# Optimization experiments

Measured on AMD Instinct MI355X. Metric: run time of the kernel, lower is better.

Reference implementation:

```python
import jax, jax.numpy as jnp
import numpy as np

H, E, V, MAXLEN, PAD = 8, 256, 1024, 64, 0


def _ln(x, g, b, eps):
    m = jnp.mean(x, -1, keepdims=True)
    v = jnp.mean((x - m) ** 2, -1, keepdims=True)
    return (x - m) / jnp.sqrt(v + eps) * g + b


def _get_pos(max_len, emb_dim):
    # replicates SVTISDPA.get_pos (sinusoidal, freq built via cumprod)
    half = emb_dim // 2
    freq = jnp.full((half,), 10000.0 ** (-1.0 / half), dtype=jnp.float32).at[0].set(1.0)
    freq = jnp.cumprod(freq)
    phase = jnp.arange(max_len, dtype=jnp.float32)[:, None] * freq[None, :]
    pe = jnp.zeros((max_len, emb_dim), dtype=jnp.float32)
    pe = pe.at[:, 0::2].set(jnp.sin(phase)).at[:, 1::2].set(jnp.cos(phase))
    return pe


def setup_inputs() -> dict:
    key = jax.random.key(0)
    ks = jax.random.split(key, 4)
    char_code = jax.random.randint(ks[0], (512, 64), 0, V)  # [B, max_len]
    emb_w = (jax.random.normal(ks[1], (V, E), dtype=jnp.float32) * 0.05).at[PAD].set(0.0)
    qkv_w = jax.random.normal(ks[2], (3 * E * H, E), dtype=jnp.float32) * 0.05
    fc_w = jax.random.normal(ks[3], (E, E * H), dtype=jnp.float32) * 0.05
    return {
        'char_code': char_code,
        'emb_w': emb_w,
        'qkv_w': qkv_w,
        'fc_w': fc_w,
        'fc_b': jnp.zeros((E,), jnp.float32),
        'sdpa_ln_g': jnp.ones((E,), jnp.float32),
        'sdpa_ln_b': jnp.zeros((E,), jnp.float32),
        'ff_ln_g': jnp.ones((E,), jnp.float32),
        'ff_ln_b': jnp.zeros((E,), jnp.float32),
        'bn_g': jnp.ones((E,), jnp.float32),
        'bn_b': jnp.zeros((E,), jnp.float32),
        'max_len': 64,
    }


def reference(char_code, emb_w, qkv_w, fc_w, fc_b, sdpa_ln_g, sdpa_ln_b,
              ff_ln_g, ff_ln_b, bn_g, bn_b, max_len):
    temp = E ** 0.5
    pos = _get_pos(MAXLEN, E)

    def qkv(x):
        y = (x @ qkv_w.T).reshape(x.shape[0], H, 3 * E)
        return y[..., :E], y[..., E:2 * E], y[..., 2 * E:]

    cq, ck, cv = qkv(emb_w)   # each [V, H, E]
    pq, pk, pv = qkv(pos)     # each [L, H, E]

    char_qk = jnp.einsum('vhe,whe->hvw', cq, ck) / temp          # [H,V,V]
    char_qk = char_qk.at[:, :, PAD].set(-1e9)
    pos_qk = jnp.einsum('lhe,mhe->hlm', pq, pk) / temp           # [H,L,L]
    char_pos_qk = (jnp.einsum('vhe,lhe->hvl', cq, pk)
                   + jnp.einsum('lhe,vhe->hvl', pq, ck)) / temp  # [H,V,L]

    c = char_code[:, :max_len]  # [B,M]
    M = max_len
    # sim[b,h,i,j] = char_qk[h,c_bi,c_bj] + char_pos_qk[h,c_bi,j] + pos_qk[h,i,j]
    sim = (char_qk[:, c[:, :, None], c[:, None, :]]
           + char_pos_qk[:, c, :M]).transpose(1, 0, 2, 3) \
          + pos_qk[None, :, :M, :M]                              # [B,H,M,M]
    attn = jax.nn.softmax(sim, axis=-1)

    not_mask = (c != PAD).astype(sim.dtype)                      # [B,M]
    n_words = jnp.sum(not_mask, -1)                              # [B]
    pooled = jnp.einsum('bm,bhmj->bhj', not_mask, attn) / n_words[:, None, None]

    v = cv[c].transpose(0, 2, 1, 3) + pv.transpose(1, 0, 2)[None, :, :M]  # [B,H,M,E]
    out = jnp.einsum('bhm,bhme->bhe', pooled, v).reshape(c.shape[0], H * E)
    out = _ln(out @ fc_w.T + fc_b, sdpa_ln_g, sdpa_ln_b, 1e-5)
    # FeedForward.forward returns layer_norm(x) (residual branch is dead code)
    out = _ln(out, ff_ln_g, ff_ln_b, 1e-6) + out
    return _ln(out, bn_g, bn_b, 1e-5)
```

## Files before the change

### kernel.cpp

```cpp
#include <hip/hip_runtime.h>
#include <math.h>

typedef unsigned short u16;
typedef __attribute__((ext_vector_type(4))) float f32x4;
typedef __attribute__((ext_vector_type(8))) short s16x8;
typedef __attribute__((ext_vector_type(4))) unsigned short u16x4;
typedef __attribute__((ext_vector_type(8))) unsigned short u16x8;

__device__ __forceinline__ u16 f2b(float f) {
  union { float f; unsigned u; } v; v.f = f;
  return (u16)((v.u + 0x7fffu + ((v.u >> 16) & 1u)) >> 16);
}
__device__ __forceinline__ float b2f(u16 b) {
  union { unsigned u; float f; } v; v.u = ((unsigned)b) << 16;
  return v.f;
}

__global__ __launch_bounds__(256) void prep_kernel(
    const float* __restrict__ emb, const float* __restrict__ qkv,
    const float* __restrict__ fc,
    u16* __restrict__ emb_bf, u16* __restrict__ qkvw_bf, u16* __restrict__ fcx,
    u16* __restrict__ pe)
{
  const int bid = blockIdx.x;
  if (bid < 2304) {
    const int i = bid * 256 + threadIdx.x;
    if (i < 65536) {
      f32x4 v = *(const f32x4*)&emb[(size_t)i * 4];
      u16x4 o = { f2b(v[0]), f2b(v[1]), f2b(v[2]), f2b(v[3]) };
      *(u16x4*)&emb_bf[(size_t)i * 4] = o;
    } else if (i < 458752) {
      const int off = i - 65536;
      f32x4 v = *(const f32x4*)&qkv[(size_t)off * 4];
      u16x4 o = { f2b(v[0]), f2b(v[1]), f2b(v[2]), f2b(v[3]) };
      *(u16x4*)&qkvw_bf[(size_t)off * 4] = o;
    } else {
      const int off4 = (i - 458752) * 4;
      const int row = off4 >> 11, col = off4 & 2047;
      f32x4 v = *(const f32x4*)&fc[(size_t)off4];
      u16x4 o = { f2b(v[0]), f2b(v[1]), f2b(v[2]), f2b(v[3]) };
      *(u16x4*)&fcx[(size_t)row * 2560 + col] = o;
    }
  } else {
    const int t = threadIdx.x;
    const int m = (bid - 2304) * 2 + (t >> 7);
    const int k = t & 127;
    float sv = 0.f, cv = 0.f;
    if (m < 64) {
      double f = pow(10000.0, -(double)k / 128.0);
      float ph = (float)m * (float)f;
      sv = sinf(ph); cv = cosf(ph);
    }
    pe[m * 256 + 2 * k]     = f2b(sv);
    pe[m * 256 + 2 * k + 1] = f2b(cv);
  }
}

__global__ __launch_bounds__(256) void gemm128(
    const u16* __restrict__ emb, const u16* __restrict__ pe,
    const u16* __restrict__ B,
    u16* __restrict__ Ccq, u16* __restrict__ Cpq)
{
  __shared__ __align__(16) u16 As[128 * 64];
  __shared__ __align__(16) u16 Bs[128 * 64];
  const int ytile = blockIdx.y;
  const u16* A; u16* C; int m0;
  if (ytile < 8) { A = emb; C = Ccq; m0 = ytile * 128; }
  else           { A = pe;  C = Cpq; m0 = 0; }
  const int n0 = blockIdx.x * 128;
  const int tid = threadIdx.x;
  const int w = tid >> 6, l = tid & 63, hi = l >> 4, lo = l & 15;
  const int wr = (w >> 1) * 64, wc = (w & 1) * 64;
  const int srow = tid >> 3, scol = (tid & 7) * 8;
  f32x4 acc[4][4] = {};
  for (int k0 = 0; k0 < 256; k0 += 64) {
    __syncthreads();
    #pragma unroll
    for (int q = 0; q < 4; ++q) {
      const int row = q * 32 + srow;
      const int sidx = row * 64 + (scol ^ ((row & 7) << 3));
      *(u16x8*)&As[sidx] = *(const u16x8*)&A[(long)(m0 + row) * 256 + k0 + scol];
      *(u16x8*)&Bs[sidx] = *(const u16x8*)&B[(long)(n0 + row) * 256 + k0 + scol];
    }
    __syncthreads();
    #pragma unroll
    for (int kk = 0; kk < 2; ++kk) {
      s16x8 a[4], bf[4];
      #pragma unroll
      for (int m = 0; m < 4; ++m) {
        const int ar = wr + m * 16 + lo;
        a[m] = *(const s16x8*)&As[ar * 64 + ((hi * 8 + kk * 32) ^ ((ar & 7) << 3))];
      }
      #pragma unroll
      for (int n = 0; n < 4; ++n) {
        const int br = wc + n * 16 + lo;
        bf[n] = *(const s16x8*)&Bs[br * 64 + ((hi * 8 + kk * 32) ^ ((br & 7) << 3))];
      }
      #pragma unroll
      for (int m = 0; m < 4; ++m)
        #pragma unroll
        for (int n = 0; n < 4; ++n)
          acc[m][n] = __builtin_amdgcn_mfma_f32_16x16x32_bf16(a[m], bf[n], acc[m][n], 0, 0, 0);
    }
  }
  #pragma unroll
  for (int m = 0; m < 4; ++m)
    #pragma unroll
    for (int n = 0; n < 4; ++n)
      #pragma unroll
      for (int r = 0; r < 4; ++r)
        C[(long)(m0 + wr + m * 16 + hi * 4 + r) * 6144 + n0 + wc + n * 16 + lo] = f2b(acc[m][n][r]);
}

__global__ __launch_bounds__(256) void gemm_bf(
    const u16* __restrict__ A, int lda, long sA,
    const u16* __restrict__ B, int ldb, long sB,
    float* __restrict__ C, int ldc, long sC, int K)
{
  __shared__ __align__(16) u16 As[64 * 64];
  __shared__ __align__(16) u16 Bs[64 * 64];
  const int z = blockIdx.z;
  A += (long)z * sA;  B += (long)z * sB;
  const int m0 = blockIdx.y * 64, n0 = blockIdx.x * 64;
  const int tid = threadIdx.x;
  const int srow = tid >> 2, sq = tid & 3;
  const int w = tid >> 6, l = tid & 63, hi = l >> 4, lo = l & 15;
  f32x4 acc[4] = {};
  for (int k0 = 0; k0 < K; k0 += 64) {
    __syncthreads();
    #pragma unroll
    for (int p = 0; p < 2; ++p) {
      const int col = sq * 16 + p * 8;
      const int sidx = srow * 64 + (col ^ ((srow & 7) << 3));
      *(u16x8*)&As[sidx] = *(const u16x8*)&A[(long)(m0 + srow) * lda + k0 + col];
      *(u16x8*)&Bs[sidx] = *(const u16x8*)&B[(long)(n0 + srow) * ldb + k0 + col];
    }
    __syncthreads();
    #pragma unroll
    for (int kk = 0; kk < 2; ++kk) {
      const int arow = w * 16 + lo;
      s16x8 a = *(const s16x8*)&As[arow * 64 + ((hi * 8 + kk * 32) ^ ((arow & 7) << 3))];
      #pragma unroll
      for (int n = 0; n < 4; ++n) {
        const int brow = n * 16 + lo;
        s16x8 bfr = *(const s16x8*)&Bs[brow * 64 + ((hi * 8 + kk * 32) ^ ((brow & 7) << 3))];
        acc[n] = __builtin_amdgcn_mfma_f32_16x16x32_bf16(a, bfr, acc[n], 0, 0, 0);
      }
    }
  }
  const long zoff = (long)z * sC;
  #pragma unroll
  for (int n = 0; n < 4; ++n)
    #pragma unroll
    for (int r = 0; r < 4; ++r)
      C[zoff + (long)(m0 + w * 16 + hi * 4 + r) * ldc + n0 + n * 16 + lo] = acc[n][r];
}

__global__ __launch_bounds__(256) void tables_kernel(
    const u16* __restrict__ cqkv, const u16* __restrict__ pqkv,
    const u16* __restrict__ fcx,
    u16* __restrict__ cpqk, u16* __restrict__ pqk, u16* __restrict__ pvfc)
{
  __shared__ __align__(16) u16 As1[64 * 64], Bs1[64 * 64];
  __shared__ __align__(16) u16 As2[64 * 64], Bs2[64 * 64];
  const int blk = blockIdx.x;
  const u16 *A1, *A2 = nullptr, *B1, *B2 = nullptr;
  u16* C; int lda, ldb, ldc, m0; bool dual = false;
  if (blk < 128) {
    const int h = blk & 7, mt = blk >> 3;
    A1 = cqkv + h * 768 + 256; A2 = cqkv + h * 768;
    B1 = pqkv + h * 768;       B2 = pqkv + h * 768 + 256;
    lda = 6144; ldb = 6144; C = cpqk + (long)h * 65536; ldc = 64;
    m0 = mt * 64; dual = true;
  } else if (blk < 136) {
    const int h = blk - 128;
    A1 = pqkv + h * 768; B1 = pqkv + h * 768 + 256;
    lda = 6144; ldb = 6144; C = pqk + h * 4096; ldc = 64; m0 = 0;
  } else {
    const int idx = blk - 136, h = idx & 7, mt = idx >> 3;
    A1 = fcx + h * 256; B1 = pqkv + 512 + h * 768;
    lda = 2560; ldb = 6144; C = pvfc + h * 64; ldc = 2560; m0 = mt * 64;
  }
  const int tid = threadIdx.x;
  const int srow = tid >> 2, sq = tid & 3;
  const int w = tid >> 6, l = tid & 63, hi = l >> 4, lo = l & 15;
  f32x4 acc[4] = {};
  for (int k0 = 0; k0 < 256; k0 += 64) {
    __syncthreads();
    #pragma unroll
    for (int p = 0; p < 2; ++p) {
      const int col = sq * 16 + p * 8;
      const int sidx = srow * 64 + (col ^ ((srow & 7) << 3));
      *(u16x8*)&As1[sidx] = *(const u16x8*)&A1[(long)(m0 + srow) * lda + k0 + col];
      *(u16x8*)&Bs1[sidx] = *(const u16x8*)&B1[(long)srow * ldb + k0 + col];
      if (dual) {
        *(u16x8*)&As2[sidx] = *(const u16x8*)&A2[(long)(m0 + srow) * lda + k0 + col];
        *(u16x8*)&Bs2[sidx] = *(const u16x8*)&B2[(long)srow * ldb + k0 + col];
      }
    }
    __syncthreads();
    #pragma unroll
    for (int kk = 0; kk < 2; ++kk) {
      const int arow = w * 16 + lo;
      const int aidx = arow * 64 + ((hi * 8 + kk * 32) ^ ((arow & 7) << 3));
      s16x8 a1 = *(const s16x8*)&As1[aidx];
      #pragma unroll
      for (int n = 0; n < 4; ++n) {
        const int brow = n * 16 + lo;
        const int bidx = brow * 64 + ((hi * 8 + kk * 32) ^ ((brow & 7) << 3));
        acc[n] = __builtin_amdgcn_mfma_f32_16x16x32_bf16(a1, *(const s16x8*)&Bs1[bidx], acc[n], 0, 0, 0);
      }
      if (dual) {
        s16x8 a2 = *(const s16x8*)&As2[aidx];
        #pragma unroll
        for (int n = 0; n < 4; ++n) {
          const int brow = n * 16 + lo;
          const int bidx = brow * 64 + ((hi * 8 + kk * 32) ^ ((brow & 7) << 3));
          acc[n] = __builtin_amdgcn_mfma_f32_16x16x32_bf16(a2, *(const s16x8*)&Bs2[bidx], acc[n], 0, 0, 0);
        }
      }
    }
  }
  #pragma unroll
  for (int n = 0; n < 4; ++n)
    #pragma unroll
    for (int r = 0; r < 4; ++r)
      C[(long)(m0 + w * 16 + hi * 4 + r) * ldc + n * 16 + lo] = f2b(acc[n][r]);
}

__global__ __launch_bounds__(256, 4) void attn_kernel(
    const int* __restrict__ cc, const u16* __restrict__ cqkv,
    const u16* __restrict__ cpqk, const u16* __restrict__ pqk,
    u16* __restrict__ outp)
{
  __shared__ __align__(16) u16 Ks[64 * 256];
  const int h = blockIdx.x, b = blockIdx.y;
  const int tid = threadIdx.x;
  const long hq = (long)h * 768;
  const int* ccb = cc + b * 64;

  const int srow = tid >> 2, sq = tid & 3;
  const int w = tid >> 6, l = tid & 63, hi = l >> 4, lo = l & 15;
  const int swz = (srow & 7) << 3;

  const int ci_s = ccb[srow];
  const float invn = 1.f / (float)__popcll(__ballot(ccb[l] != 0));

  const long crow = ((long)h * 1024 + ci_s) * 64;
  const long prow = (long)h * 4096 + (long)srow * 64;
  u16x8 ct0 = *(const u16x8*)&cpqk[crow + sq * 8];
  u16x8 ct1 = *(const u16x8*)&cpqk[crow + sq * 8 + 32];
  u16x8 pt0 = *(const u16x8*)&pqk[prow + sq * 8];
  u16x8 pt1 = *(const u16x8*)&pqk[prow + sq * 8 + 32];

  const long qrow = (long)ccb[w * 16 + lo] * 6144 + hq;
  s16x8 a[8];
  #pragma unroll
  for (int kk = 0; kk < 8; ++kk)
    a[kk] = *(const s16x8*)&cqkv[qrow + kk * 32 + hi * 8];

  {
    const long kbase = (long)ci_s * 6144 + hq + 256;
    u16x8 kr[8];
    #pragma unroll
    for (int p = 0; p < 8; ++p)
      kr[p] = *(const u16x8*)&cqkv[kbase + sq * 8 + p * 32];
    #pragma unroll
    for (int p = 0; p < 8; ++p)
      *(u16x8*)&Ks[srow * 256 + ((sq * 8 + p * 32) ^ swz)] = kr[p];
  }

  const long vrow = (long)ci_s * 6144 + hq + 512;
  u16x8 va[8];
  #pragma unroll
  for (int p = 0; p < 8; ++p)
    va[p] = *(const u16x8*)&cqkv[vrow + sq * 8 + p * 32];

  __syncthreads();

  f32x4 acc[4] = {};
  #pragma unroll
  for (int kk = 0; kk < 8; ++kk) {
    #pragma unroll
    for (int n = 0; n < 4; ++n) {
      const int brow = n * 16 + lo;
      s16x8 bfr = *(const s16x8*)&Ks[brow * 256 + ((hi * 8 + kk * 32) ^ ((brow & 7) << 3))];
      acc[n] = __builtin_amdgcn_mfma_f32_16x16x32_bf16(a[kk], bfr, acc[n], 0, 0, 0);
    }
  }
  __syncthreads();

  *(u16x8*)&Ks[srow * 64 + ((sq * 8) ^ swz)]             = ct0;
  *(u16x8*)&Ks[srow * 64 + ((sq * 8 + 32) ^ swz)]        = ct1;
  *(u16x8*)&Ks[4096 + srow * 64 + ((sq * 8) ^ swz)]      = pt0;
  *(u16x8*)&Ks[4096 + srow * 64 + ((sq * 8 + 32) ^ swz)] = pt1;
  __syncthreads();

  const float scale = 0.0625f;
  int csj[4];
  #pragma unroll
  for (int n = 0; n < 4; ++n) csj[n] = ccb[n * 16 + lo];
  float ex[4][4];
  float wgt[4];
  #pragma unroll
  for (int r = 0; r < 4; ++r) {
    const int i = w * 16 + hi * 4 + r;
    const int tswz = (i & 7) << 3;
    float s[4];
    float mx = -3e38f;
    #pragma unroll
    for (int n = 0; n < 4; ++n) {
      const int j = n * 16 + lo;
      const int cidx = i * 64 + (j ^ tswz);
      float v = (acc[n][r] + b2f(Ks[cidx]) + b2f(Ks[4096 + cidx])) * scale;
      if (csj[n] == 0) v = -1e9f;
      s[n] = v;
      mx = fmaxf(mx, v);
    }
    mx = fmaxf(mx, __shfl_xor(mx, 1));
    mx = fmaxf(mx, __shfl_xor(mx, 2));
    mx = fmaxf(mx, __shfl_xor(mx, 4));
    mx = fmaxf(mx, __shfl_xor(mx, 8));
    float sum = 0.f;
    #pragma unroll
    for (int n = 0; n < 4; ++n) { const float e = __expf(s[n] - mx); ex[n][r] = e; sum += e; }
    sum += __shfl_xor(sum, 1);
    sum += __shfl_xor(sum, 2);
    sum += __shfl_xor(sum, 4);
    sum += __shfl_xor(sum, 8);
    wgt[r] = (ccb[i] != 0 ? 1.f : 0.f) / sum;
  }
  float* poolpF = (float*)&Ks[8192];
  #pragma unroll
  for (int n = 0; n < 4; ++n) {
    float cp = ex[n][0] * wgt[0] + ex[n][1] * wgt[1] + ex[n][2] * wgt[2] + ex[n][3] * wgt[3];
    cp += __shfl_xor(cp, 16);
    cp += __shfl_xor(cp, 32);
    if (hi == 0) poolpF[w * 64 + n * 16 + lo] = cp;
  }
  __syncthreads();

  const float pl = (poolpF[l] + poolpF[64 + l] + poolpF[128 + l] + poolpF[192 + l]) * invn;
  if (tid < 64)
    outp[(long)b * 2560 + 2048 + h * 64 + tid] = f2b(pl);
  __syncthreads();

  #pragma unroll
  for (int p = 0; p < 8; ++p)
    *(u16x8*)&Ks[srow * 256 + ((sq * 8 + p * 32) ^ swz)] = va[p];
  __syncthreads();

  float o = 0.f;
  #pragma unroll
  for (int j = 0; j < 64; ++j)
    o += __shfl(pl, j) * b2f(Ks[j * 256 + (tid ^ ((j & 7) << 3))]);
  outp[(long)b * 2560 + h * 256 + tid] = f2b(o);
}

__global__ __launch_bounds__(256) void ln_chain(
    const float* __restrict__ xp, const float* __restrict__ fcb,
    const float* __restrict__ g1, const float* __restrict__ b1,
    const float* __restrict__ g2, const float* __restrict__ b2,
    const float* __restrict__ g3, const float* __restrict__ b3,
    float* __restrict__ out)
{
  __shared__ float red[4];
  const int b = blockIdx.x, t = threadIdx.x;
  const long idx = (long)b * 256 + t;
  float v = xp[idx] + xp[idx + 131072] + xp[idx + 262144] + xp[idx + 393216] + fcb[t];

  auto bsum = [&](float val) -> float {
    #pragma unroll
    for (int o = 32; o; o >>= 1) val += __shfl_down(val, o);
    __syncthreads();
    if ((t & 63) == 0) red[t >> 6] = val;
    __syncthreads();
    return red[0] + red[1] + red[2] + red[3];
  };

  float mean = bsum(v) * (1.f / 256.f);
  float d = v - mean;
  float var = bsum(d * d) * (1.f / 256.f);
  const float y1 = d * rsqrtf(var + 1e-5f) * g1[t] + b1[t];

  mean = bsum(y1) * (1.f / 256.f);
  d = y1 - mean;
  var = bsum(d * d) * (1.f / 256.f);
  const float y2 = d * rsqrtf(var + 1e-6f) * g2[t] + b2[t] + y1;

  mean = bsum(y2) * (1.f / 256.f);
  d = y2 - mean;
  var = bsum(d * d) * (1.f / 256.f);
  out[idx] = d * rsqrtf(var + 1e-5f) * g3[t] + b3[t];
}

extern "C" void kernel_launch(void* const* d_in, const int* in_sizes, int n_in,
                              void* d_out, int out_size, void* d_ws, size_t ws_size,
                              hipStream_t stream) {
  (void)in_sizes; (void)n_in; (void)out_size; (void)ws_size;
  const int*   cc    = (const int*)  d_in[0];
  const float* emb_w = (const float*)d_in[1];
  const float* qkv_w = (const float*)d_in[2];
  const float* fc_w  = (const float*)d_in[3];
  const float* fc_b  = (const float*)d_in[4];
  const float* sg    = (const float*)d_in[5];
  const float* sb    = (const float*)d_in[6];
  const float* fg    = (const float*)d_in[7];
  const float* fb    = (const float*)d_in[8];
  const float* bg    = (const float*)d_in[9];
  const float* bbv   = (const float*)d_in[10];
  float* out = (float*)d_out;

  char* p = (char*)d_ws;
  u16* pe_pad  = (u16*)p;  p += (size_t)128 * 256 * 2;
  u16* emb_bf  = (u16*)p;  p += (size_t)1024 * 256 * 2;
  u16* qkvw_bf = (u16*)p;  p += (size_t)6144 * 256 * 2;
  u16* fcx     = (u16*)p;  p += (size_t)256 * 2560 * 2;
  u16* cqkv_bf = (u16*)p;  p += (size_t)1024 * 6144 * 2;
  u16* pqkv_bf = (u16*)p;  p += (size_t)128 * 6144 * 2;
  u16* cpqk16  = (u16*)p;  p += (size_t)8 * 1024 * 64 * 2;
  u16* pqk16   = (u16*)p;  p += (size_t)8 * 64 * 64 * 2;
  u16* sdpa_bf = (u16*)p;  p += (size_t)512 * 2560 * 2;
  float* fco   = (float*)p; p += (size_t)4 * 512 * 256 * 4;

  prep_kernel<<<dim3(2368), dim3(256), 0, stream>>>(
      emb_w, qkv_w, fc_w, emb_bf, qkvw_bf, fcx, pe_pad);

  gemm128<<<dim3(48, 9), dim3(256), 0, stream>>>(
      emb_bf, pe_pad, qkvw_bf, cqkv_bf, pqkv_bf);

  tables_kernel<<<dim3(168), dim3(256), 0, stream>>>(
      cqkv_bf, pqkv_bf, fcx, cpqk16, pqk16, fcx + 2048);

  attn_kernel<<<dim3(8, 512), dim3(256), 0, stream>>>(
      cc, cqkv_bf, cpqk16, pqk16, sdpa_bf);

  gemm_bf<<<dim3(4, 8, 4), dim3(256), 0, stream>>>(
      sdpa_bf, 2560, 640, fcx, 2560, 640, fco, 256, (long)512 * 256, 640);

  ln_chain<<<dim3(512), dim3(256), 0, stream>>>(fco, fc_b, sg, sb, fg, fb, bg, bbv, out);
}
```

Before: 86.92 us.

## Coalesce tile loads and pre-sum positional score tables in attention kernel

Global-to-shared loads in the GEMM kernels and the attention kernel now have 8 threads cover a contiguous 128-byte row segment, replacing the old interleaved 4-thread pattern, so memory accesses coalesce better. The attention kernel stages the char codes in shared memory, adds the char-position and position-position bias tiles into a single bf16 tile before the softmax, and keeps pooled weights in a dedicated shared array instead of broadcasting them with shuffles. Summing the two bias tiles in bf16 adds an extra rounding step, and the dedicated arrays increase shared memory use per block.

```diff
diff --git a/kernel.cpp b/kernel.cpp
--- a/kernel.cpp
+++ b/kernel.cpp
@@ -123,17 +123,17 @@
   A += (long)z * sA;  B += (long)z * sB;
   const int m0 = blockIdx.y * 64, n0 = blockIdx.x * 64;
   const int tid = threadIdx.x;
-  const int srow = tid >> 2, sq = tid & 3;
+  const int r8 = tid >> 3, s8t = (tid & 7) * 8;
   const int w = tid >> 6, l = tid & 63, hi = l >> 4, lo = l & 15;
   f32x4 acc[4] = {};
   for (int k0 = 0; k0 < K; k0 += 64) {
     __syncthreads();
     #pragma unroll
-    for (int p = 0; p < 2; ++p) {
-      const int col = sq * 16 + p * 8;
-      const int sidx = srow * 64 + (col ^ ((srow & 7) << 3));
-      *(u16x8*)&As[sidx] = *(const u16x8*)&A[(long)(m0 + srow) * lda + k0 + col];
-      *(u16x8*)&Bs[sidx] = *(const u16x8*)&B[(long)(n0 + srow) * ldb + k0 + col];
+    for (int q = 0; q < 2; ++q) {
+      const int row = q * 32 + r8;
+      const int sidx = row * 64 + (s8t ^ ((row & 7) << 3));
+      *(u16x8*)&As[sidx] = *(const u16x8*)&A[(long)(m0 + row) * lda + k0 + s8t];
+      *(u16x8*)&Bs[sidx] = *(const u16x8*)&B[(long)(n0 + row) * ldb + k0 + s8t];
     }
     __syncthreads();
     #pragma unroll
@@ -182,20 +182,20 @@
     lda = 2560; ldb = 6144; C = pvfc + h * 64; ldc = 2560; m0 = mt * 64;
   }
   const int tid = threadIdx.x;
-  const int srow = tid >> 2, sq = tid & 3;
+  const int r8 = tid >> 3, s8t = (tid & 7) * 8;
   const int w = tid >> 6, l = tid & 63, hi = l >> 4, lo = l & 15;
   f32x4 acc[4] = {};
   for (int k0 = 0; k0 < 256; k0 += 64) {
     __syncthreads();
     #pragma unroll
-    for (int p = 0; p < 2; ++p) {
-      const int col = sq * 16 + p * 8;
-      const int sidx = srow * 64 + (col ^ ((srow & 7) << 3));
-      *(u16x8*)&As1[sidx] = *(const u16x8*)&A1[(long)(m0 + srow) * lda + k0 + col];
-      *(u16x8*)&Bs1[sidx] = *(const u16x8*)&B1[(long)srow * ldb + k0 + col];
+    for (int q = 0; q < 2; ++q) {
+      const int row = q * 32 + r8;
+      const int sidx = row * 64 + (s8t ^ ((row & 7) << 3));
+      *(u16x8*)&As1[sidx] = *(const u16x8*)&A1[(long)(m0 + row) * lda + k0 + s8t];
+      *(u16x8*)&Bs1[sidx] = *(const u16x8*)&B1[(long)row * ldb + k0 + s8t];
       if (dual) {
-        *(u16x8*)&As2[sidx] = *(const u16x8*)&A2[(long)(m0 + srow) * lda + k0 + col];
-        *(u16x8*)&Bs2[sidx] = *(const u16x8*)&B2[(long)srow * ldb + k0 + col];
+        *(u16x8*)&As2[sidx] = *(const u16x8*)&A2[(long)(m0 + row) * lda + k0 + s8t];
+        *(u16x8*)&Bs2[sidx] = *(const u16x8*)&B2[(long)row * ldb + k0 + s8t];
       }
     }
     __syncthreads();
@@ -234,48 +234,52 @@
     u16* __restrict__ outp)
 {
   __shared__ __align__(16) u16 Ks[64 * 256];
+  __shared__ int   cs[64];
+  __shared__ float poolp[4][64];
+  __shared__ float pooled[64];
   const int h = blockIdx.x, b = blockIdx.y;
   const int tid = threadIdx.x;
   const long hq = (long)h * 768;
-  const int* ccb = cc + b * 64;
-
-  const int srow = tid >> 2, sq = tid & 3;
+
   const int w = tid >> 6, l = tid & 63, hi = l >> 4, lo = l & 15;
-  const int swz = (srow & 7) << 3;
-
-  const int ci_s = ccb[srow];
-  const float invn = 1.f / (float)__popcll(__ballot(ccb[l] != 0));
-
-  const long crow = ((long)h * 1024 + ci_s) * 64;
-  const long prow = (long)h * 4096 + (long)srow * 64;
-  u16x8 ct0 = *(const u16x8*)&cpqk[crow + sq * 8];
-  u16x8 ct1 = *(const u16x8*)&cpqk[crow + sq * 8 + 32];
-  u16x8 pt0 = *(const u16x8*)&pqk[prow + sq * 8];
-  u16x8 pt1 = *(const u16x8*)&pqk[prow + sq * 8 + 32];
-
-  const long qrow = (long)ccb[w * 16 + lo] * 6144 + hq;
+  const int r8 = tid >> 3, s8t = (tid & 7) * 8;
+  const int rb = r8 + 32;
+
+  if (tid < 64) cs[tid] = cc[b * 64 + tid];
+  __syncthreads();
+  const float invn = 1.f / (float)__popcll(__ballot(cs[l] != 0));
+
+  const int ca = cs[r8], cb = cs[rb];
+  const long rowa = (long)ca * 6144 + hq;
+  const long rowb = (long)cb * 6144 + hq;
+
+  u16x8 kr[8];
+  #pragma unroll
+  for (int p = 0; p < 4; ++p) {
+    kr[p]     = *(const u16x8*)&cqkv[rowa + 256 + p * 64 + s8t];
+    kr[p + 4] = *(const u16x8*)&cqkv[rowb + 256 + p * 64 + s8t];
+  }
+  u16x8 vr[8];
+  #pragma unroll
+  for (int p = 0; p < 4; ++p) {
+    vr[p]     = *(const u16x8*)&cqkv[rowa + 512 + p * 64 + s8t];
+    vr[p + 4] = *(const u16x8*)&cqkv[rowb + 512 + p * 64 + s8t];
+  }
+  u16x8 cta = *(const u16x8*)&cpqk[((long)h * 1024 + ca) * 64 + s8t];
+  u16x8 ctb = *(const u16x8*)&cpqk[((long)h * 1024 + cb) * 64 + s8t];
+  u16x8 pta = *(const u16x8*)&pqk[(long)h * 4096 + (long)r8 * 64 + s8t];
+  u16x8 ptb = *(const u16x8*)&pqk[(long)h * 4096 + (long)rb * 64 + s8t];
+  const long qrow = (long)cs[w * 16 + lo] * 6144 + hq;
   s16x8 a[8];
   #pragma unroll
   for (int kk = 0; kk < 8; ++kk)
     a[kk] = *(const s16x8*)&cqkv[qrow + kk * 32 + hi * 8];
 
-  {
-    const long kbase = (long)ci_s * 6144 + hq + 256;
-    u16x8 kr[8];
-    #pragma unroll
-    for (int p = 0; p < 8; ++p)
-      kr[p] = *(const u16x8*)&cqkv[kbase + sq * 8 + p * 32];
-    #pragma unroll
-    for (int p = 0; p < 8; ++p)
-      *(u16x8*)&Ks[srow * 256 + ((sq * 8 + p * 32) ^ swz)] = kr[p];
-  }
-
-  const long vrow = (long)ci_s * 6144 + hq + 512;
-  u16x8 va[8];
-  #pragma unroll
-  for (int p = 0; p < 8; ++p)
-    va[p] = *(const u16x8*)&cqkv[vrow + sq * 8 + p * 32];
-
+  #pragma unroll
+  for (int p = 0; p < 4; ++p) {
+    *(u16x8*)&Ks[r8 * 256 + ((p * 64 + s8t) ^ ((r8 & 7) << 3))] = kr[p];
+    *(u16x8*)&Ks[rb * 256 + ((p * 64 + s8t) ^ ((rb & 7) << 3))] = kr[p + 4];
+  }
   __syncthreads();
 
   f32x4 acc[4] = {};
@@ -290,16 +294,22 @@
   }
   __syncthreads();
 
-  *(u16x8*)&Ks[srow * 64 + ((sq * 8) ^ swz)]             = ct0;
-  *(u16x8*)&Ks[srow * 64 + ((sq * 8 + 32) ^ swz)]        = ct1;
-  *(u16x8*)&Ks[4096 + srow * 64 + ((sq * 8) ^ swz)]      = pt0;
-  *(u16x8*)&Ks[4096 + srow * 64 + ((sq * 8 + 32) ^ swz)] = pt1;
+  {
+    u16x8 t0, t1;
+    #pragma unroll
+    for (int d = 0; d < 8; ++d) {
+      t0[d] = f2b(b2f(cta[d]) + b2f(pta[d]));
+      t1[d] = f2b(b2f(ctb[d]) + b2f(ptb[d]));
+    }
+    *(u16x8*)&Ks[r8 * 64 + (s8t ^ ((r8 & 7) << 3))] = t0;
+    *(u16x8*)&Ks[rb * 64 + (s8t ^ ((rb & 7) << 3))] = t1;
+  }
   __syncthreads();
 
   const float scale = 0.0625f;
   int csj[4];
   #pragma unroll
-  for (int n = 0; n < 4; ++n) csj[n] = ccb[n * 16 + lo];
+  for (int n = 0; n < 4; ++n) csj[n] = cs[n * 16 + lo];
   float ex[4][4];
   float wgt[4];
   #pragma unroll
@@ -311,8 +321,7 @@
     #pragma unroll
     for (int n = 0; n < 4; ++n) {
       const int j = n * 16 + lo;
-      const int cidx = i * 64 + (j ^ tswz);
-      float v = (acc[n][r] + b2f(Ks[cidx]) + b2f(Ks[4096 + cidx])) * scale;
+      float v = (acc[n][r] + b2f(Ks[i * 64 + (j ^ tswz)])) * scale;
       if (csj[n] == 0) v = -1e9f;
       s[n] = v;
       mx = fmaxf(mx, v);
@@ -328,32 +337,33 @@
     sum += __shfl_xor(sum, 2);
     sum += __shfl_xor(sum, 4);
     sum += __shfl_xor(sum, 8);
-    wgt[r] = (ccb[i] != 0 ? 1.f : 0.f) / sum;
-  }
-  float* poolpF = (float*)&Ks[8192];
+    wgt[r] = (cs[i] != 0 ? 1.f : 0.f) / sum;
+  }
   #pragma unroll
   for (int n = 0; n < 4; ++n) {
     float cp = ex[n][0] * wgt[0] + ex[n][1] * wgt[1] + ex[n][2] * wgt[2] + ex[n][3] * wgt[3];
     cp += __shfl_xor(cp, 16);
     cp += __shfl_xor(cp, 32);
-    if (hi == 0) poolpF[w * 64 + n * 16 + lo] = cp;
-  }
-  __syncthreads();
-
-  const float pl = (poolpF[l] + poolpF[64 + l] + poolpF[128 + l] + poolpF[192 + l]) * invn;
-  if (tid < 64)
+    if (hi == 0) poolp[w][n * 16 + lo] = cp;
+  }
+  __syncthreads();
+
+  if (tid < 64) {
+    const float pl = (poolp[0][tid] + poolp[1][tid] + poolp[2][tid] + poolp[3][tid]) * invn;
+    pooled[tid] = pl;
     outp[(long)b * 2560 + 2048 + h * 64 + tid] = f2b(pl);
-  __syncthreads();
-
-  #pragma unroll
-  for (int p = 0; p < 8; ++p)
-    *(u16x8*)&Ks[srow * 256 + ((sq * 8 + p * 32) ^ swz)] = va[p];
+  }
+  #pragma unroll
+  for (int p = 0; p < 4; ++p) {
+    *(u16x8*)&Ks[r8 * 256 + ((p * 64 + s8t) ^ ((r8 & 7) << 3))] = vr[p];
+    *(u16x8*)&Ks[rb * 256 + ((p * 64 + s8t) ^ ((rb & 7) << 3))] = vr[p + 4];
+  }
   __syncthreads();
 
   float o = 0.f;
   #pragma unroll
   for (int j = 0; j < 64; ++j)
-    o += __shfl(pl, j) * b2f(Ks[j * 256 + (tid ^ ((j & 7) << 3))]);
+    o += pooled[j] * b2f(Ks[j * 256 + (tid ^ ((j & 7) << 3))]);
   outp[(long)b * 2560 + h * 256 + tid] = f2b(o);
 }
 
```

After: 86.81 us. About the same (-0.1%).
